# Kernel optimization log

Hardware: AMD Instinct MI355X
Metric: run time of the kernel (lower is better)

Reference implementation:

```python
import jax, jax.numpy as jnp
import numpy as np

B, C, H, W = 8, 256, 64, 64
CM = C // 4          # mask channels (theta/phi out) = 64
CI = C - CM          # img channels = 192
EPS = 1e-5


def setup_inputs() -> dict:
    key = jax.random.key(0)
    ks = jax.random.split(key, 12)
    return {
        "x": jax.random.normal(ks[0], (B, C, H, W), dtype=jnp.float32),
        "g_w": jax.random.normal(ks[1], (C, C), dtype=jnp.float32) * 0.05,
        "g_b": jax.random.normal(ks[2], (C,), dtype=jnp.float32) * 0.01,
        "theta_w": jax.random.normal(ks[3], (CM, CM), dtype=jnp.float32) * 0.1,
        "theta_b": jax.random.normal(ks[4], (CM,), dtype=jnp.float32) * 0.01,
        "phi_w": jax.random.normal(ks[5], (CM, CI), dtype=jnp.float32) * 0.06,
        "phi_b": jax.random.normal(ks[6], (CM,), dtype=jnp.float32) * 0.01,
        "W_w": jax.random.normal(ks[7], (C, C), dtype=jnp.float32) * 0.05,
        "W_b": jax.random.normal(ks[8], (C,), dtype=jnp.float32) * 0.01,
        "bn_gamma": jax.random.normal(ks[9], (C,), dtype=jnp.float32) * 0.1 + 1.0,
        "bn_beta": jax.random.normal(ks[10], (C,), dtype=jnp.float32) * 0.01,
        "bn_mean": jax.random.normal(ks[11], (C,), dtype=jnp.float32) * 0.1,
        "bn_var": jnp.ones((C,), dtype=jnp.float32),
    }


def _conv1x1(t, w, b):
    # [B,Cin,H,W] x [Cout,Cin] -> [B,Cout,H,W]
    return jnp.einsum('bchw,oc->bohw', t, w) + b[None, :, None, None]


def _maxpool2(t):
    b, c, h, w = t.shape
    return t.reshape(b, c, h // 2, 2, w // 2, 2).max(axis=(3, 5))


def reference(x, g_w, g_b, theta_w, theta_b, phi_w, phi_b, W_w, W_b,
              bn_gamma, bn_beta, bn_mean, bn_var):
    b, c, h, w = x.shape
    ci = c // 4
    mask_ch = x[:, :ci]          # [B, C/4, H, W]
    img_ch = x[:, ci:]           # [B, 3C/4, H, W]

    # g: conv1x1 then 2x2 maxpool -> [B, C, N'] -> [B, N', C]
    g_x = _maxpool2(_conv1x1(x, g_w, g_b)).reshape(b, c, -1).transpose(0, 2, 1)
    # theta: conv1x1 on mask -> [B, N, C/4]
    theta_x = _conv1x1(mask_ch, theta_w, theta_b).reshape(b, ci, -1).transpose(0, 2, 1)
    # phi: conv1x1 on img then pool -> [B, C/4, N']
    phi_x = _maxpool2(_conv1x1(img_ch, phi_w, phi_b)).reshape(b, ci, -1)

    f = jnp.einsum('bnc,bcm->bnm', theta_x, phi_x)     # [B, N, N']
    f_div_C = jax.nn.softmax(f, axis=-1)
    y = jnp.einsum('bnm,bmc->bnc', f_div_C, g_x)       # [B, N, C]
    y = y.transpose(0, 2, 1).reshape(b, c, h, w)

    W_y = _conv1x1(y, W_w, W_b)
    # BatchNorm (inference form with running stats)
    inv = jax.lax.rsqrt(bn_var + EPS)
    W_y = (W_y - bn_mean[None, :, None, None]) * (inv * bn_gamma)[None, :, None, None] \
          + bn_beta[None, :, None, None]
    return W_y + x
```

## Files before the change

kernel.cpp:

```cpp
#include <hip/hip_runtime.h>
#include <hip/hip_bf16.h>

typedef __hip_bfloat16 bf16;
typedef unsigned short ushort;
typedef unsigned int uint;
typedef __attribute__((ext_vector_type(8))) short short8;
typedef __attribute__((ext_vector_type(4))) float f32x4;

#define Bn 8
#define Cn 256
#define Nn 4096
#define Mn 1024
#define EPSf 1e-5f

__device__ __forceinline__ float b2f(const bf16 v){ return __bfloat162float(v); }
__device__ __forceinline__ ushort f2bu(float f){
  uint u = __float_as_uint(f);
  return (ushort)((u + 0x7FFFu + ((u >> 16) & 1u)) >> 16);
}


__global__ __launch_bounds__(256) void transpose_kernel(
    const float* __restrict__ x, bf16* __restrict__ xT)
{
  __shared__ float xs[64][65];
  const int t = threadIdx.x;
  const int p0 = blockIdx.x*64, c0 = blockIdx.y*64, b = blockIdx.z;
  #pragma unroll
  for (int i = 0; i < 16; ++i) {
    int idx = t + i*256; int cl = idx >> 6, pl = idx & 63;
    xs[cl][pl] = x[((long)(b*Cn) + c0 + cl)*Nn + p0 + pl];
  }
  __syncthreads();
  ushort* xt = (ushort*)xT;
  const int ql = t & 15, quad = (t >> 4) & 3, w = t >> 6;
  #pragma unroll
  for (int i = 0; i < 2; ++i) {
    int f = w + i*4;
    int p16f = f >> 1, kcf = f & 1;
    int pl = p16f*16 + ql;
    int ch0 = kcf*32 + quad*8;
    uint u[4];
    #pragma unroll
    for (int k = 0; k < 4; ++k)
      u[k] = (uint)f2bu(xs[ch0 + 2*k][pl]) | ((uint)f2bu(xs[ch0 + 2*k + 1][pl]) << 16);
    long base = ((long)b*2048 + ((p0>>4) + p16f)*8 + (c0>>5) + kcf)*512;
    *(uint4*)(xt + base + (t & 63)*8) = make_uint4(u[0], u[1], u[2], u[3]);
  }
}

__global__ __launch_bounds__(256) void wcomb_kernel(
    const float* __restrict__ tw, const float* __restrict__ tb,
    const float* __restrict__ pw, const float* __restrict__ pb,
    const float* __restrict__ gw, const float* __restrict__ gb,
    bf16* __restrict__ Wcomb, float* __restrict__ bcomb)
{
  const int r = blockIdx.x, c = threadIdx.x;
  float v;
  if (r < 64)        v = (c < 64)  ? tw[r*64 + c]            : 0.f;
  else if (r < 128)  v = (c >= 64) ? pw[(r-64)*192 + (c-64)] : 0.f;
  else               v = gw[(r-128)*256 + c];
  ((ushort*)Wcomb)[((r>>4)*8 + (c>>5))*512 + (((c&31)>>3)*16 + (r&15))*8 + (c&7)]
      = f2bu(v);
  if (c == 0)
    bcomb[r] = (r < 64) ? tb[r] : (r < 128) ? pb[r-64] : gb[r-128];
}

__global__ __launch_bounds__(256) void wwt_kernel(
    const float* __restrict__ Ww, bf16* __restrict__ Wwt)
{
  const int r = blockIdx.x, c = threadIdx.x;
  ((ushort*)Wwt)[((r>>4)*8 + (c>>5))*512 + (((c&31)>>3)*16 + (r&15))*8 + (c&7)]
      = f2bu(Ww[r*256 + c]);
}

__global__ __launch_bounds__(256) void gemm384_kernel(
    const bf16* __restrict__ xTt, const bf16* __restrict__ Wct,
    const float* __restrict__ bcomb, bf16* __restrict__ Q,
    bf16* __restrict__ K, bf16* __restrict__ Vt)
{
  __shared__ float Pb[2][128][33];
  const int t = threadIdx.x;
  const int px = blockIdx.x, o0 = blockIdx.y*128, b = blockIdx.z;
  const int p0 = px*128;
  const int lane = t & 63, w = t >> 6;
  const int ql = lane & 15, quad = lane >> 4;
  const int wm = (w & 1)*64, wn = (w >> 1)*64;
  const ushort* xu = (const ushort*)xTt;
  const ushort* wu = (const ushort*)Wct;

  const ushort* aB[4]; const ushort* bB[4];
  #pragma unroll
  for (int mi = 0; mi < 4; ++mi)
    aB[mi] = xu + (((long)b*256 + px*8 + (wm>>4) + mi)*8)*512 + lane*8;
  #pragma unroll
  for (int ni = 0; ni < 4; ++ni)
    bB[ni] = wu + ((long)(((o0 + wn)>>4) + ni)*8)*512 + lane*8;

  f32x4 acc[4][4];
  #pragma unroll
  for (int i = 0; i < 4; ++i)
    #pragma unroll
    for (int j = 0; j < 4; ++j) acc[i][j] = (f32x4){0.f,0.f,0.f,0.f};

  short8 aX[4], bX[4], aY[4], bY[4];
  #pragma unroll
  for (int i = 0; i < 4; ++i) {
    aX[i] = *(const short8*)(aB[i]);
    bX[i] = *(const short8*)(bB[i]);
    aY[i] = *(const short8*)(aB[i] + 512);
    bY[i] = *(const short8*)(bB[i] + 512);
  }
  #pragma unroll
  for (int kc2 = 0; kc2 < 4; ++kc2) {
    #pragma unroll
    for (int mi = 0; mi < 4; ++mi)
      #pragma unroll
      for (int ni = 0; ni < 4; ++ni)
        acc[mi][ni] = __builtin_amdgcn_mfma_f32_16x16x32_bf16(aX[mi], bX[ni], acc[mi][ni], 0, 0, 0);
    if (kc2 < 3) {
      #pragma unroll
      for (int i = 0; i < 4; ++i) {
        aX[i] = *(const short8*)(aB[i] + (kc2*2 + 2)*512);
        bX[i] = *(const short8*)(bB[i] + (kc2*2 + 2)*512);
      }
    }
    #pragma unroll
    for (int mi = 0; mi < 4; ++mi)
      #pragma unroll
      for (int ni = 0; ni < 4; ++ni)
        acc[mi][ni] = __builtin_amdgcn_mfma_f32_16x16x32_bf16(aY[mi], bY[ni], acc[mi][ni], 0, 0, 0);
    if (kc2 < 3) {
      #pragma unroll
      for (int i = 0; i < 4; ++i) {
        aY[i] = *(const short8*)(aB[i] + (kc2*2 + 3)*512);
        bY[i] = *(const short8*)(bB[i] + (kc2*2 + 3)*512);
      }
    }
  }

  float bias[4];
  #pragma unroll
  for (int ni = 0; ni < 4; ++ni) bias[ni] = bcomb[o0 + wn + ni*16 + ql];

  if (o0 == 0 && wn == 0) {
    #pragma unroll
    for (int mi = 0; mi < 4; ++mi)
      #pragma unroll
      for (int ni = 0; ni < 4; ++ni)
        #pragma unroll
        for (int r = 0; r < 4; ++r) {
          int p = p0 + wm + mi*16 + quad*4 + r;
          Q[((long)(b*Nn) + p)*64 + ni*16 + ql] = __float2bfloat16(acc[mi][ni][r] + bias[ni]);
        }
  }
  __syncthreads();
  if (o0 != 0 || wn == 64) {
    int g = w & 1;
    #pragma unroll
    for (int mi = 0; mi < 4; ++mi)
      #pragma unroll
      for (int ni = 0; ni < 4; ++ni) {
        float a0 = acc[mi][ni][0] + bias[ni], a1 = acc[mi][ni][1] + bias[ni];
        float a2 = acc[mi][ni][2] + bias[ni], a3 = acc[mi][ni][3] + bias[ni];
        int o = wn + ni*16 + ql;
        int wp = mi*8 + quad*2;
        Pb[g][o][wp]     = fmaxf(a0, a1);
        Pb[g][o][wp + 1] = fmaxf(a2, a3);
      }
  }
  __syncthreads();
  if (o0 == 0) {
    int wp = t & 31, og = t >> 5;
    ushort kv[8];
    #pragma unroll
    for (int j = 0; j < 8; ++j) {
      int o = 64 + og*8 + j;
      kv[j] = f2bu(fmaxf(Pb[0][o][wp], Pb[1][o][wp]));
    }
    long kidx = ((long)(b*64) + px*2 + (wp>>4))*1024 + (og>>2)*512
              + ((og&3)*16 + (wp&15))*8;
    *(uint4*)((ushort*)K + kidx) = *(uint4*)kv;
  } else {
    int ol = t >> 1, wp0 = (t & 1)*16;
    ushort vv[16];
    #pragma unroll
    for (int j = 0; j < 16; ++j)
      vv[j] = f2bu(fmaxf(Pb[0][ol][wp0 + j], Pb[1][ol][wp0 + j]));
    int n = (o0 - 128) + ol;
    long vbase = (long)(b)*262144 + (px>>1)*16384 + (n>>4)*1024 + (px&1)*512;
    ushort* dst0 = (ushort*)Vt + vbase + ((wp0>>3)*16 + (n&15))*8;
    *(uint4*)dst0         = *(uint4*)(vv);
    *(uint4*)(dst0 + 128) = *(uint4*)(vv + 8);
  }
}

__global__ __launch_bounds__(512) void attn_kernel(
    const bf16* __restrict__ Q, const bf16* __restrict__ K, const bf16* __restrict__ Vt,
    bf16* __restrict__ Y)
{
  __shared__ __align__(16) ushort Ps[2][64*68];
  __shared__ float l_sh[2][64];

  const int t = threadIdx.x;
  const int b = blockIdx.y, q0 = blockIdx.x*64;
  const int lane = t & 63, w = t >> 6;
  const int ql = lane & 15, quad = lane >> 4;
  const int rt = w & 3;
  const int kh = w >> 2;
  const int rh = (w & 1)*32;
  const int cq = (w >> 1)*64;
  const ushort* Qu = (const ushort*)Q;
  const ushort* Ku = (const ushort*)K;
  const ushort* Vu = (const ushort*)Vt;

  const long qrow = (long)(b*Nn) + q0 + rt*16 + ql;
  short8 aQ0 = *(const short8*)(Qu + qrow*64 + quad*8);
  short8 aQ1 = *(const short8*)(Qu + qrow*64 + 32 + quad*8);

  const ushort* kfp = Ku + ((long)(b*64) + kh*2)*1024 + lane*8;
  const ushort* vfp = Vu + (long)(b)*262144 + (cq>>4)*1024 + lane*8;

  float lrow[4];
  #pragma unroll
  for (int r = 0; r < 4; ++r) lrow[r] = 0.f;

  f32x4 acc[2][4];
  #pragma unroll
  for (int mi = 0; mi < 2; ++mi)
    #pragma unroll
    for (int ci = 0; ci < 4; ++ci) acc[mi][ci] = (f32x4){0.f,0.f,0.f,0.f};

  short8 kf[4], vf[8];
  auto LD_K = [&](int mt){
    #pragma unroll
    for (int ct = 0; ct < 2; ++ct)
      #pragma unroll
      for (int hf = 0; hf < 2; ++hf)
        kf[ct*2+hf] = *(const short8*)(kfp + mt*4096 + ct*1024 + hf*512);
  };
  auto LD_V = [&](int mt){
    #pragma unroll
    for (int ci = 0; ci < 4; ++ci)
      #pragma unroll
      for (int hf = 0; hf < 2; ++hf)
        vf[ci*2+hf] = *(const short8*)(vfp + mt*16384 + ci*1024 + hf*512);
  };
  auto QK = [&](int sel){
    #pragma unroll
    for (int ct = 0; ct < 2; ++ct) {
      int kb = kh*32 + ct*16;
      f32x4 s = (f32x4){0.f,0.f,0.f,0.f};
      s = __builtin_amdgcn_mfma_f32_16x16x32_bf16(aQ0, kf[ct*2],   s, 0, 0, 0);
      s = __builtin_amdgcn_mfma_f32_16x16x32_bf16(aQ1, kf[ct*2+1], s, 0, 0, 0);
      #pragma unroll
      for (int r = 0; r < 4; ++r) {
        float e = __expf(s[r]);
        lrow[r] += e;
        Ps[sel][(rt*16 + quad*4 + r)*68 + kb + ql] = f2bu(e);
      }
    }
  };
  auto PV = [&](int sel){
    short8 aP0[2], aP1[2];
    #pragma unroll
    for (int mi = 0; mi < 2; ++mi) {
      aP0[mi] = *(const short8*)(&Ps[sel][(rh + mi*16 + ql)*68 + quad*8]);
      aP1[mi] = *(const short8*)(&Ps[sel][(rh + mi*16 + ql)*68 + 32 + quad*8]);
    }
    #pragma unroll
    for (int ci = 0; ci < 4; ++ci)
      #pragma unroll
      for (int mi = 0; mi < 2; ++mi) {
        acc[mi][ci] = __builtin_amdgcn_mfma_f32_16x16x32_bf16(aP0[mi], vf[ci*2],   acc[mi][ci], 0, 0, 0);
        acc[mi][ci] = __builtin_amdgcn_mfma_f32_16x16x32_bf16(aP1[mi], vf[ci*2+1], acc[mi][ci], 0, 0, 0);
      }
  };

  LD_K(0);
  LD_V(0);
  QK(0);
  LD_K(1);
  __syncthreads();

  for (int mt = 1; mt < 16; ++mt) {
    PV((mt-1)&1);
    LD_V(mt);
    QK(mt&1);
    LD_K((mt+1)&15);
    __syncthreads();
  }
  PV(1);

  #pragma unroll
  for (int r = 0; r < 4; ++r)
    #pragma unroll
    for (int off = 1; off < 16; off <<= 1)
      lrow[r] += __shfl_xor(lrow[r], off, 64);
  if (ql == 0) {
    #pragma unroll
    for (int r = 0; r < 4; ++r) l_sh[kh][rt*16 + quad*4 + r] = lrow[r];
  }
  __syncthreads();
  ushort* Yu = (ushort*)Y;
  #pragma unroll
  for (int mi = 0; mi < 2; ++mi)
    #pragma unroll
    for (int r = 0; r < 4; ++r) {
      int row = rh + mi*16 + quad*4 + r;
      float inv = 1.f / (l_sh[0][row] + l_sh[1][row]);
      int n = q0 + row;
      #pragma unroll
      for (int ci = 0; ci < 4; ++ci) {
        int c = cq + ci*16 + ql;
        long idx = (((long)b*256 + (n>>4))*8 + (c>>5))*512
                 + (((c&31)>>3)*16 + (n&15))*8 + (c&7);
        Yu[idx] = f2bu(acc[mi][ci][r]*inv);
      }
    }
}

__global__ __launch_bounds__(256) void wconv_kernel(
    const bf16* __restrict__ Yt, const bf16* __restrict__ Wwt, const float* __restrict__ Wb,
    const float* __restrict__ gamma, const float* __restrict__ beta,
    const float* __restrict__ mean, const float* __restrict__ var,
    const float* __restrict__ x, float* __restrict__ out)
{
  __shared__ float ssc[128], ssh[128];
  const int t = threadIdx.x;
  const int n0 = blockIdx.x*128, o0 = blockIdx.y*128, b = blockIdx.z;
  const int lane = t & 63, w = t >> 6;
  const int ql = lane & 15, quad = lane >> 4;
  const int wm = (w & 1)*64, wn = (w >> 1)*64;

  if (t < 128) {
    int o = o0 + t;
    float sc = gamma[o] * rsqrtf(var[o] + EPSf);
    ssc[t] = sc;
    ssh[t] = (Wb[o] - mean[o])*sc + beta[o];
  }

  const ushort* aB[4]; const ushort* bB[4];
  #pragma unroll
  for (int mi = 0; mi < 4; ++mi)
    aB[mi] = (const ushort*)Wwt + ((long)(((o0 + wm)>>4) + mi)*8)*512 + lane*8;
  #pragma unroll
  for (int ni = 0; ni < 4; ++ni)
    bB[ni] = (const ushort*)Yt + (((long)b*256 + ((n0 + wn)>>4) + ni)*8)*512 + lane*8;

  f32x4 acc[4][4];
  #pragma unroll
  for (int i = 0; i < 4; ++i)
    #pragma unroll
    for (int j = 0; j < 4; ++j) acc[i][j] = (f32x4){0.f,0.f,0.f,0.f};

  short8 aX[4], bX[4], aY[4], bY[4];
  #pragma unroll
  for (int i = 0; i < 4; ++i) {
    aX[i] = *(const short8*)(aB[i]);
    bX[i] = *(const short8*)(bB[i]);
    aY[i] = *(const short8*)(aB[i] + 512);
    bY[i] = *(const short8*)(bB[i] + 512);
  }
  #pragma unroll
  for (int kc2 = 0; kc2 < 4; ++kc2) {
    #pragma unroll
    for (int mi = 0; mi < 4; ++mi)
      #pragma unroll
      for (int ni = 0; ni < 4; ++ni)
        acc[mi][ni] = __builtin_amdgcn_mfma_f32_16x16x32_bf16(aX[mi], bX[ni], acc[mi][ni], 0, 0, 0);
    if (kc2 < 3) {
      #pragma unroll
      for (int i = 0; i < 4; ++i) {
        aX[i] = *(const short8*)(aB[i] + (kc2*2 + 2)*512);
        bX[i] = *(const short8*)(bB[i] + (kc2*2 + 2)*512);
      }
    }
    #pragma unroll
    for (int mi = 0; mi < 4; ++mi)
      #pragma unroll
      for (int ni = 0; ni < 4; ++ni)
        acc[mi][ni] = __builtin_amdgcn_mfma_f32_16x16x32_bf16(aY[mi], bY[ni], acc[mi][ni], 0, 0, 0);
    if (kc2 < 3) {
      #pragma unroll
      for (int i = 0; i < 4; ++i) {
        aY[i] = *(const short8*)(aB[i] + (kc2*2 + 3)*512);
        bY[i] = *(const short8*)(bB[i] + (kc2*2 + 3)*512);
      }
    }
  }
  __syncthreads();
  #pragma unroll
  for (int mi = 0; mi < 4; ++mi)
    #pragma unroll
    for (int r = 0; r < 4; ++r) {
      int ol = wm + mi*16 + quad*4 + r;
      int o = o0 + ol;
      float sc = ssc[ol], sh = ssh[ol];
      #pragma unroll
      for (int ni = 0; ni < 4; ++ni) {
        int n = n0 + wn + ni*16 + ql;
        long gidx = ((long)(b*Cn + o))*Nn + n;
        out[gidx] = acc[mi][ni][r]*sc + sh + x[gidx];
      }
    }
}

extern "C" void kernel_launch(void* const* d_in, const int* in_sizes, int n_in,
                              void* d_out, int out_size, void* d_ws, size_t ws_size,
                              hipStream_t stream)
{
  const float* x       = (const float*)d_in[0];
  const float* g_w     = (const float*)d_in[1];
  const float* g_b     = (const float*)d_in[2];
  const float* theta_w = (const float*)d_in[3];
  const float* theta_b = (const float*)d_in[4];
  const float* phi_w   = (const float*)d_in[5];
  const float* phi_b   = (const float*)d_in[6];
  const float* W_w     = (const float*)d_in[7];
  const float* W_b     = (const float*)d_in[8];
  const float* bn_g    = (const float*)d_in[9];
  const float* bn_b    = (const float*)d_in[10];
  const float* bn_m    = (const float*)d_in[11];
  const float* bn_v    = (const float*)d_in[12];
  float* out = (float*)d_out;

  bf16* wsb = (bf16*)d_ws;
  bf16* xTt   = wsb;
  bf16* Yt    = wsb;
  bf16* Q     = wsb + 8388608;
  bf16* K     = wsb + 10485760;
  bf16* Vt    = wsb + 11010048;
  bf16* Wct   = wsb + 13107200;
  float* bcomb = (float*)(wsb + 13205504);
  bf16* Wwt   = wsb + 13206272;

  transpose_kernel<<<dim3(64, 4, Bn), 256, 0, stream>>>(x, xTt);
  wcomb_kernel<<<dim3(384), 256, 0, stream>>>(theta_w, theta_b, phi_w, phi_b, g_w, g_b, Wct, bcomb);
  wwt_kernel<<<dim3(256), 256, 0, stream>>>(W_w, Wwt);
  gemm384_kernel<<<dim3(32, 3, Bn), 256, 0, stream>>>(xTt, Wct, bcomb, Q, K, Vt);
  attn_kernel<<<dim3(64, Bn), 512, 0, stream>>>(Q, K, Vt, Yt);
  wconv_kernel<<<dim3(32, 2, Bn), 256, 0, stream>>>(Yt, Wwt, W_b, bn_g, bn_b, bn_m, bn_v, x, out);
}
```

Before: 172.0 us.

## Enlarge attention query tile to 128 rows and redistribute warp work

The attention kernel now handles 128 query rows per block instead of 64, halving the grid. Each warp computes QK for its own 16 rows across the full 64-key tile, and PV for 32 rows by 128 channels. Each K/V tile loaded from global memory is therefore reused across twice as many queries, and the cross-warp row-sum reduction is no longer needed. In exchange, per-thread registers roughly double (accumulators, K and V fragments), LDS use grows, and the 256-block grid may leave some compute units underused.

```diff
diff --git a/kernel.cpp b/kernel.cpp
--- a/kernel.cpp
+++ b/kernel.cpp
@@ -195,61 +195,58 @@
   }
 }
 
-__global__ __launch_bounds__(512) void attn_kernel(
+__global__ __launch_bounds__(512, 2) void attn_kernel(
     const bf16* __restrict__ Q, const bf16* __restrict__ K, const bf16* __restrict__ Vt,
     bf16* __restrict__ Y)
 {
-  __shared__ __align__(16) ushort Ps[2][64*68];
-  __shared__ float l_sh[2][64];
+  __shared__ __align__(16) ushort Ps[2][128*68];
+  __shared__ float l_sh[128];
 
   const int t = threadIdx.x;
-  const int b = blockIdx.y, q0 = blockIdx.x*64;
+  const int b = blockIdx.y, q0 = blockIdx.x*128;
   const int lane = t & 63, w = t >> 6;
   const int ql = lane & 15, quad = lane >> 4;
-  const int rt = w & 3;
-  const int kh = w >> 2;
-  const int rh = (w & 1)*32;
-  const int cq = (w >> 1)*64;
+  const int rg = w & 3;
+  const int cg = w >> 2;
   const ushort* Qu = (const ushort*)Q;
   const ushort* Ku = (const ushort*)K;
   const ushort* Vu = (const ushort*)Vt;
 
-  const long qrow = (long)(b*Nn) + q0 + rt*16 + ql;
+  const long qrow = (long)(b*Nn) + q0 + w*16 + ql;
   short8 aQ0 = *(const short8*)(Qu + qrow*64 + quad*8);
   short8 aQ1 = *(const short8*)(Qu + qrow*64 + 32 + quad*8);
 
-  const ushort* kfp = Ku + ((long)(b*64) + kh*2)*1024 + lane*8;
-  const ushort* vfp = Vu + (long)(b)*262144 + (cq>>4)*1024 + lane*8;
+  const ushort* kfp = Ku + (long)(b*64)*1024 + lane*8;
+  const ushort* vfp = Vu + (long)(b)*262144 + (cg*8)*1024 + lane*8;
 
   float lrow[4];
   #pragma unroll
   for (int r = 0; r < 4; ++r) lrow[r] = 0.f;
 
-  f32x4 acc[2][4];
+  f32x4 acc[2][8];
   #pragma unroll
   for (int mi = 0; mi < 2; ++mi)
     #pragma unroll
-    for (int ci = 0; ci < 4; ++ci) acc[mi][ci] = (f32x4){0.f,0.f,0.f,0.f};
-
-  short8 kf[4], vf[8];
+    for (int ci = 0; ci < 8; ++ci) acc[mi][ci] = (f32x4){0.f,0.f,0.f,0.f};
+
+  short8 kf[8], vf[16];
   auto LD_K = [&](int mt){
     #pragma unroll
-    for (int ct = 0; ct < 2; ++ct)
+    for (int ct = 0; ct < 4; ++ct)
       #pragma unroll
       for (int hf = 0; hf < 2; ++hf)
         kf[ct*2+hf] = *(const short8*)(kfp + mt*4096 + ct*1024 + hf*512);
   };
   auto LD_V = [&](int mt){
     #pragma unroll
-    for (int ci = 0; ci < 4; ++ci)
+    for (int ci = 0; ci < 8; ++ci)
       #pragma unroll
       for (int hf = 0; hf < 2; ++hf)
         vf[ci*2+hf] = *(const short8*)(vfp + mt*16384 + ci*1024 + hf*512);
   };
   auto QK = [&](int sel){
     #pragma unroll
-    for (int ct = 0; ct < 2; ++ct) {
-      int kb = kh*32 + ct*16;
+    for (int ct = 0; ct < 4; ++ct) {
       f32x4 s = (f32x4){0.f,0.f,0.f,0.f};
       s = __builtin_amdgcn_mfma_f32_16x16x32_bf16(aQ0, kf[ct*2],   s, 0, 0, 0);
       s = __builtin_amdgcn_mfma_f32_16x16x32_bf16(aQ1, kf[ct*2+1], s, 0, 0, 0);
@@ -257,7 +254,7 @@
       for (int r = 0; r < 4; ++r) {
         float e = __expf(s[r]);
         lrow[r] += e;
-        Ps[sel][(rt*16 + quad*4 + r)*68 + kb + ql] = f2bu(e);
+        Ps[sel][(w*16 + quad*4 + r)*68 + ct*16 + ql] = f2bu(e);
       }
     }
   };
@@ -265,11 +262,11 @@
     short8 aP0[2], aP1[2];
     #pragma unroll
     for (int mi = 0; mi < 2; ++mi) {
-      aP0[mi] = *(const short8*)(&Ps[sel][(rh + mi*16 + ql)*68 + quad*8]);
-      aP1[mi] = *(const short8*)(&Ps[sel][(rh + mi*16 + ql)*68 + 32 + quad*8]);
-    }
-    #pragma unroll
-    for (int ci = 0; ci < 4; ++ci)
+      aP0[mi] = *(const short8*)(&Ps[sel][(rg*32 + mi*16 + ql)*68 + quad*8]);
+      aP1[mi] = *(const short8*)(&Ps[sel][(rg*32 + mi*16 + ql)*68 + 32 + quad*8]);
+    }
+    #pragma unroll
+    for (int ci = 0; ci < 8; ++ci)
       #pragma unroll
       for (int mi = 0; mi < 2; ++mi) {
         acc[mi][ci] = __builtin_amdgcn_mfma_f32_16x16x32_bf16(aP0[mi], vf[ci*2],   acc[mi][ci], 0, 0, 0);
@@ -299,7 +296,7 @@
       lrow[r] += __shfl_xor(lrow[r], off, 64);
   if (ql == 0) {
     #pragma unroll
-    for (int r = 0; r < 4; ++r) l_sh[kh][rt*16 + quad*4 + r] = lrow[r];
+    for (int r = 0; r < 4; ++r) l_sh[w*16 + quad*4 + r] = lrow[r];
   }
   __syncthreads();
   ushort* Yu = (ushort*)Y;
@@ -307,12 +304,12 @@
   for (int mi = 0; mi < 2; ++mi)
     #pragma unroll
     for (int r = 0; r < 4; ++r) {
-      int row = rh + mi*16 + quad*4 + r;
-      float inv = 1.f / (l_sh[0][row] + l_sh[1][row]);
+      int row = rg*32 + mi*16 + quad*4 + r;
+      float inv = 1.f / l_sh[row];
       int n = q0 + row;
       #pragma unroll
-      for (int ci = 0; ci < 4; ++ci) {
-        int c = cq + ci*16 + ql;
+      for (int ci = 0; ci < 8; ++ci) {
+        int c = cg*128 + ci*16 + ql;
         long idx = (((long)b*256 + (n>>4))*8 + (c>>5))*512
                  + (((c&31)>>3)*16 + (n&15))*8 + (c&7);
         Yu[idx] = f2bu(acc[mi][ci][r]*inv);
@@ -439,6 +436,6 @@
   wcomb_kernel<<<dim3(384), 256, 0, stream>>>(theta_w, theta_b, phi_w, phi_b, g_w, g_b, Wct, bcomb);
   wwt_kernel<<<dim3(256), 256, 0, stream>>>(W_w, Wwt);
   gemm384_kernel<<<dim3(32, 3, Bn), 256, 0, stream>>>(xTt, Wct, bcomb, Q, K, Vt);
-  attn_kernel<<<dim3(64, Bn), 512, 0, stream>>>(Q, K, Vt, Yt);
+  attn_kernel<<<dim3(32, Bn), 512, 0, stream>>>(Q, K, Vt, Yt);
   wconv_kernel<<<dim3(32, 2, Bn), 256, 0, stream>>>(Yt, Wwt, W_b, bn_g, bn_b, bn_m, bn_v, x, out);
 }
```

Result: no change. 175.3 us (+1.9%).
